# Optimization experiments

Measured on AMD Instinct MI355X. Metric: run time of the kernel, lower is better.

## Reference

```python
import jax, jax.numpy as jnp
import numpy as np

BETA = 0.1
NBINS = 100
LM1 = float(np.log(0.01))   # lower histogram edge
LM2 = float(np.log(400.0))  # upper histogram edge
EPS = 1e-05


def _get_probability(x):
    # torch.histogram(x, 100, range=(lm1, lm2)): counts only in-range values,
    # right edge inclusive in last bin -- matches jnp.histogram semantics.
    h, _ = jnp.histogram(x.reshape(-1), bins=NBINS, range=(LM1, LM2))
    h = h.astype(jnp.float32) + EPS
    return h / jnp.sum(h)


def setup_inputs() -> dict:
    key = jax.random.key(0)
    k1, k2 = jax.random.split(key)
    shape = (128, 1, 512, 512)
    pred = jax.random.normal(k1, shape, dtype=jnp.float32)
    actual = jax.random.normal(k2, shape, dtype=jnp.float32)
    return {"pred": pred, "actual": actual}


def reference(pred, actual):
    # MSELoss(reduction='mean')
    mse = jnp.mean((pred - actual) ** 2)

    # KLDivLoss(reduction='batchmean', log_target=True) over 100-bin histograms;
    # input = log(p_pred), target = log(p_actual):
    #   sum(exp(t) * (t - i)) / N  with N = 100 (first dim of the histogram vec).
    p = _get_probability(pred)
    a = _get_probability(actual)
    kld = jnp.sum(a * (jnp.log(a) - jnp.log(p))) / NBINS

    return mse + BETA * kld
```

## Files before the change

kernel.cpp:

```cpp
#include <hip/hip_runtime.h>
#include <math.h>

#define NBINS 100
static constexpr float LM1f  = -4.605170185988091f;
static constexpr float LM2f  =  5.991464547107982f;
static constexpr float EPSV  = 1e-5f;
static constexpr float BETA  = 0.1f;

__global__ __launch_bounds__(256) void mse_hist_kernel(
    const float4* __restrict__ pred, const float4* __restrict__ act,
    long long n4, long long ntail, const float* __restrict__ pred_s,
    const float* __restrict__ act_s,
    float* __restrict__ sumsq, unsigned int* __restrict__ hp,
    unsigned int* __restrict__ ha)
{
    __shared__ unsigned int sh[4][2 * NBINS];
    const int wave = threadIdx.x >> 6;

    for (int i = threadIdx.x; i < 4 * 2 * NBINS; i += blockDim.x)
        ((unsigned int*)sh)[i] = 0u;
    __syncthreads();

    const float scale = (float)NBINS / (LM2f - LM1f);
    unsigned int* mh = sh[wave];

    float acc = 0.f;
    long long idx    = (long long)blockIdx.x * blockDim.x + threadIdx.x;
    long long stride = (long long)gridDim.x * blockDim.x;

    for (long long i = idx; i < n4; i += stride) {
        float4 p = pred[i];
        float4 a = act[i];
        float d0 = p.x - a.x, d1 = p.y - a.y, d2 = p.z - a.z, d3 = p.w - a.w;
        acc += d0 * d0 + d1 * d1 + d2 * d2 + d3 * d3;

        float vals[8] = {p.x, p.y, p.z, p.w, a.x, a.y, a.z, a.w};
        #pragma unroll
        for (int j = 0; j < 8; ++j) {
            float x = vals[j];
            if (x >= LM1f && x <= LM2f) {
                int b = (int)((x - LM1f) * scale);
                if (b > NBINS - 1) b = NBINS - 1;
                atomicAdd(&mh[(j >= 4 ? NBINS : 0) + b], 1u);
            }
        }
    }

    if (blockIdx.x == 0 && threadIdx.x == 0) {
        for (long long i = 0; i < ntail; ++i) {
            float p = pred_s[4 * n4 + i];
            float a = act_s[4 * n4 + i];
            float d = p - a;
            acc += d * d;
            float v2[2] = {p, a};
            for (int j = 0; j < 2; ++j) {
                float x = v2[j];
                if (x >= LM1f && x <= LM2f) {
                    int b = (int)((x - LM1f) * scale);
                    if (b > NBINS - 1) b = NBINS - 1;
                    atomicAdd(&mh[(j == 1 ? NBINS : 0) + b], 1u);
                }
            }
        }
    }
    __syncthreads();

    for (int i = threadIdx.x; i < 2 * NBINS; i += blockDim.x) {
        unsigned int s = sh[0][i] + sh[1][i] + sh[2][i] + sh[3][i];
        if (s) {
            if (i < NBINS) atomicAdd(&hp[i], s);
            else           atomicAdd(&ha[i - NBINS], s);
        }
    }

    for (int off = 32; off > 0; off >>= 1)
        acc += __shfl_down(acc, off);
    __shared__ float wsum[4];
    if ((threadIdx.x & 63) == 0) wsum[wave] = acc;
    __syncthreads();
    if (threadIdx.x == 0)
        atomicAdd(sumsq, wsum[0] + wsum[1] + wsum[2] + wsum[3]);
}

__global__ __launch_bounds__(128) void finalize_kernel(
    const float* __restrict__ sumsq, const unsigned int* __restrict__ hp,
    const unsigned int* __restrict__ ha, float* __restrict__ out, float n_elems)
{
    const int t = threadIdx.x;
    float hpv = 0.f, hav = 0.f;
    if (t < NBINS) {
        hpv = (float)hp[t] + EPSV;
        hav = (float)ha[t] + EPSV;
    }

    float sp = hpv, sa = hav;
    for (int off = 32; off > 0; off >>= 1) {
        sp += __shfl_down(sp, off);
        sa += __shfl_down(sa, off);
    }
    __shared__ float shp[2], sha[2];
    if ((t & 63) == 0) { shp[t >> 6] = sp; sha[t >> 6] = sa; }
    __syncthreads();
    const float tot_p = shp[0] + shp[1];
    const float tot_a = sha[0] + sha[1];

    float term = 0.f;
    if (t < NBINS) {
        float pv = hpv / tot_p;
        float av = hav / tot_a;
        term = av * (logf(av) - logf(pv));
    }
    for (int off = 32; off > 0; off >>= 1)
        term += __shfl_down(term, off);
    __shared__ float st[2];
    if ((t & 63) == 0) st[t >> 6] = term;
    __syncthreads();
    if (t == 0) {
        float kld = (st[0] + st[1]) / (float)NBINS;
        out[0] = sumsq[0] / n_elems + BETA * kld;
    }
}

extern "C" void kernel_launch(void* const* d_in, const int* in_sizes, int n_in,
                              void* d_out, int out_size, void* d_ws, size_t ws_size,
                              hipStream_t stream) {
    const float* pred = (const float*)d_in[0];
    const float* act  = (const float*)d_in[1];
    const long long n  = (long long)in_sizes[0];
    const long long n4 = n / 4;
    const long long ntail = n - 4 * n4;

    float*        sumsq = (float*)d_ws;
    unsigned int* hp    = (unsigned int*)d_ws + 1;
    unsigned int* ha    = (unsigned int*)d_ws + 1 + NBINS;

    hipMemsetAsync(d_ws, 0, (1 + 2 * NBINS) * sizeof(unsigned int), stream);

    const int blocks = 2048;
    mse_hist_kernel<<<blocks, 256, 0, stream>>>(
        (const float4*)pred, (const float4*)act, n4, ntail, pred, act,
        sumsq, hp, ha);

    finalize_kernel<<<1, 128, 0, stream>>>(sumsq, hp, ha, (float*)d_out, (float)n);
}
```

Measured before the change: 100.2 us.

## Replicate shared histogram into 16 lane-interleaved copies and process 8 elements per thread

Measured after the change: 94.20 us. -6.0%, faster.

```diff
diff --git a/kernel.cpp b/kernel.cpp
--- a/kernel.cpp
+++ b/kernel.cpp
@@ -2,81 +2,102 @@
 #include <math.h>
 
 #define NBINS 100
+#define NCOPY 16
 static constexpr float LM1f  = -4.605170185988091f;
 static constexpr float LM2f  =  5.991464547107982f;
 static constexpr float EPSV  = 1e-5f;
 static constexpr float BETA  = 0.1f;
 
 __global__ __launch_bounds__(256) void mse_hist_kernel(
-    const float4* __restrict__ pred, const float4* __restrict__ act,
-    long long n4, long long ntail, const float* __restrict__ pred_s,
-    const float* __restrict__ act_s,
+    const float4* __restrict__ pred4, const float4* __restrict__ act4,
+    const float* __restrict__ pred_s, const float* __restrict__ act_s,
+    long long n,
     float* __restrict__ sumsq, unsigned int* __restrict__ hp,
     unsigned int* __restrict__ ha)
 {
-    __shared__ unsigned int sh[4][2 * NBINS];
-    const int wave = threadIdx.x >> 6;
-
-    for (int i = threadIdx.x; i < 4 * 2 * NBINS; i += blockDim.x)
-        ((unsigned int*)sh)[i] = 0u;
+    __shared__ unsigned int sh[2 * NBINS * NCOPY];
+    for (int i = threadIdx.x; i < 2 * NBINS * NCOPY; i += blockDim.x)
+        sh[i] = 0u;
     __syncthreads();
 
+    const int   c     = threadIdx.x & (NCOPY - 1);
     const float scale = (float)NBINS / (LM2f - LM1f);
-    unsigned int* mh = sh[wave];
+    unsigned int* __restrict__ shp = sh;
+    unsigned int* __restrict__ sha = sh + NBINS * NCOPY;
 
     float acc = 0.f;
+    const long long n4 = n >> 2;
+    const long long n8 = n4 >> 1;
     long long idx    = (long long)blockIdx.x * blockDim.x + threadIdx.x;
     long long stride = (long long)gridDim.x * blockDim.x;
 
-    for (long long i = idx; i < n4; i += stride) {
-        float4 p = pred[i];
-        float4 a = act[i];
-        float d0 = p.x - a.x, d1 = p.y - a.y, d2 = p.z - a.z, d3 = p.w - a.w;
-        acc += d0 * d0 + d1 * d1 + d2 * d2 + d3 * d3;
+#define HVAL(xv, base) do {                                       \
+        float x_ = (xv);                                          \
+        if (x_ >= LM1f && x_ <= LM2f) {                           \
+            int b_ = (int)((x_ - LM1f) * scale);                  \
+            if (b_ > NBINS - 1) b_ = NBINS - 1;                   \
+            atomicAdd(&base[b_ * NCOPY + c], 1u);                 \
+        }                                                         \
+    } while (0)
 
-        float vals[8] = {p.x, p.y, p.z, p.w, a.x, a.y, a.z, a.w};
-        #pragma unroll
-        for (int j = 0; j < 8; ++j) {
-            float x = vals[j];
-            if (x >= LM1f && x <= LM2f) {
-                int b = (int)((x - LM1f) * scale);
-                if (b > NBINS - 1) b = NBINS - 1;
-                atomicAdd(&mh[(j >= 4 ? NBINS : 0) + b], 1u);
-            }
-        }
+    for (long long i = idx; i < n8; i += stride) {
+        float4 p0 = pred4[2 * i];
+        float4 p1 = pred4[2 * i + 1];
+        float4 a0 = act4[2 * i];
+        float4 a1 = act4[2 * i + 1];
+
+        float d;
+        d = p0.x - a0.x; acc += d * d;
+        d = p0.y - a0.y; acc += d * d;
+        d = p0.z - a0.z; acc += d * d;
+        d = p0.w - a0.w; acc += d * d;
+        d = p1.x - a1.x; acc += d * d;
+        d = p1.y - a1.y; acc += d * d;
+        d = p1.z - a1.z; acc += d * d;
+        d = p1.w - a1.w; acc += d * d;
+
+        HVAL(p0.x, shp); HVAL(p0.y, shp); HVAL(p0.z, shp); HVAL(p0.w, shp);
+        HVAL(p1.x, shp); HVAL(p1.y, shp); HVAL(p1.z, shp); HVAL(p1.w, shp);
+        HVAL(a0.x, sha); HVAL(a0.y, sha); HVAL(a0.z, sha); HVAL(a0.w, sha);
+        HVAL(a1.x, sha); HVAL(a1.y, sha); HVAL(a1.z, sha); HVAL(a1.w, sha);
     }
 
     if (blockIdx.x == 0 && threadIdx.x == 0) {
-        for (long long i = 0; i < ntail; ++i) {
-            float p = pred_s[4 * n4 + i];
-            float a = act_s[4 * n4 + i];
-            float d = p - a;
-            acc += d * d;
-            float v2[2] = {p, a};
-            for (int j = 0; j < 2; ++j) {
-                float x = v2[j];
-                if (x >= LM1f && x <= LM2f) {
-                    int b = (int)((x - LM1f) * scale);
-                    if (b > NBINS - 1) b = NBINS - 1;
-                    atomicAdd(&mh[(j == 1 ? NBINS : 0) + b], 1u);
-                }
-            }
+        for (long long j = 2 * n8; j < n4; ++j) {
+            float4 p = pred4[j], a = act4[j];
+            float d;
+            d = p.x - a.x; acc += d * d;
+            d = p.y - a.y; acc += d * d;
+            d = p.z - a.z; acc += d * d;
+            d = p.w - a.w; acc += d * d;
+            HVAL(p.x, shp); HVAL(p.y, shp); HVAL(p.z, shp); HVAL(p.w, shp);
+            HVAL(a.x, sha); HVAL(a.y, sha); HVAL(a.z, sha); HVAL(a.w, sha);
+        }
+        for (long long j = 4 * n4; j < n; ++j) {
+            float p = pred_s[j], a = act_s[j];
+            float d = p - a; acc += d * d;
+            HVAL(p, shp);
+            HVAL(a, sha);
         }
     }
+#undef HVAL
     __syncthreads();
 
-    for (int i = threadIdx.x; i < 2 * NBINS; i += blockDim.x) {
-        unsigned int s = sh[0][i] + sh[1][i] + sh[2][i] + sh[3][i];
+    for (int bin = threadIdx.x; bin < 2 * NBINS; bin += blockDim.x) {
+        unsigned int s = 0;
+        const unsigned int* p = sh + bin * NCOPY;
+        #pragma unroll
+        for (int k = 0; k < NCOPY; ++k) s += p[k];
         if (s) {
-            if (i < NBINS) atomicAdd(&hp[i], s);
-            else           atomicAdd(&ha[i - NBINS], s);
+            if (bin < NBINS) atomicAdd(&hp[bin], s);
+            else             atomicAdd(&ha[bin - NBINS], s);
         }
     }
 
     for (int off = 32; off > 0; off >>= 1)
         acc += __shfl_down(acc, off);
     __shared__ float wsum[4];
-    if ((threadIdx.x & 63) == 0) wsum[wave] = acc;
+    if ((threadIdx.x & 63) == 0) wsum[threadIdx.x >> 6] = acc;
     __syncthreads();
     if (threadIdx.x == 0)
         atomicAdd(sumsq, wsum[0] + wsum[1] + wsum[2] + wsum[3]);
@@ -126,9 +147,7 @@
                               hipStream_t stream) {
     const float* pred = (const float*)d_in[0];
     const float* act  = (const float*)d_in[1];
-    const long long n  = (long long)in_sizes[0];
-    const long long n4 = n / 4;
-    const long long ntail = n - 4 * n4;
+    const long long n = (long long)in_sizes[0];
 
     float*        sumsq = (float*)d_ws;
     unsigned int* hp    = (unsigned int*)d_ws + 1;
@@ -138,7 +157,7 @@
 
     const int blocks = 2048;
     mse_hist_kernel<<<blocks, 256, 0, stream>>>(
-        (const float4*)pred, (const float4*)act, n4, ntail, pred, act,
+        (const float4*)pred, (const float4*)act, pred, act, n,
         sumsq, hp, ha);
 
     finalize_kernel<<<1, 128, 0, stream>>>(sumsq, hp, ha, (float*)d_out, (float)n);
```
